# Kernel tuning notes

Measured on AMD Instinct MI355X. Metric: run time of the kernel, lower is better.

Reference implementation:

```python
import jax, jax.numpy as jnp
import numpy as np

B, N, C, H = 2, 2048, 1024, 16
D = C // H
SCALE = D ** -0.5


def setup_inputs() -> dict:
    key = jax.random.key(0)
    ks = jax.random.split(key, 5)
    x = jax.random.normal(ks[0], (B, N, C), dtype=jnp.float32)
    # causal mask, broadcast over batch: True = attend
    attention_mask = jnp.broadcast_to(jnp.tril(jnp.ones((N, N), dtype=bool)), (B, N, N))
    w_qkv = jax.random.normal(ks[1], (3 * C, C), dtype=jnp.float32) * (C ** -0.5)
    b_qkv = jax.random.normal(ks[2], (3 * C,), dtype=jnp.float32) * 0.02
    w_proj = jax.random.normal(ks[3], (C, C), dtype=jnp.float32) * (C ** -0.5)
    b_proj = jax.random.normal(ks[4], (C,), dtype=jnp.float32) * 0.02
    return {"x": x, "attention_mask": attention_mask, "w_qkv": w_qkv,
            "b_qkv": b_qkv, "w_proj": w_proj, "b_proj": b_proj}


def reference(x, attention_mask, w_qkv, b_qkv, w_proj, b_proj):
    b, n, c = x.shape
    qkv = x @ w_qkv.T + b_qkv                      # [B,N,3C]
    qkv = qkv.reshape(b, n, 3, H, D).transpose(2, 0, 3, 1, 4)  # [3,B,H,N,D]
    q, k, v = qkv[0], qkv[1], qkv[2]
    dots = jnp.einsum('bhid,bhjd->bhij', q, k) * SCALE
    mask_value = -jnp.finfo(dots.dtype).max
    dots = jnp.where(attention_mask[:, None, :, :], dots, mask_value)
    attn = jax.nn.softmax(dots.astype(jnp.float32), axis=-1).astype(dots.dtype)
    out = jnp.einsum('bhij,bhjd->bhid', attn, v)   # [B,H,N,D]
    # NOTE: original code reshapes WITHOUT transposing heads back - faithful.
    out = out.reshape(b, n, c)
    return out @ w_proj.T + b_proj
```

## Files before the change

kernel.cpp:

```cpp
#include <hip/hip_runtime.h>
#include <hip/hip_bf16.h>
#include <stdint.h>

#define SL_F 0.18033688011112043f

typedef unsigned short u16;
typedef unsigned int u32;
typedef __attribute__((ext_vector_type(8))) short bf16x8;
typedef __attribute__((ext_vector_type(4))) float f32x4;

__device__ __forceinline__ u16 f2bf(float f) {
    union { float f; u32 u; } v; v.f = f;
    return (u16)((v.u + 0x7fffu + ((v.u >> 16) & 1u)) >> 16);
}
__device__ __forceinline__ u32 pack2bf(float a, float b) {
    union { __hip_bfloat162 h; u32 u; } p;
    p.h = __float22bfloat162_rn(make_float2(a, b));
    return p.u;
}

__device__ __forceinline__ void gl_lds16(const u16* g, u16* l) {
    __builtin_amdgcn_global_load_lds(
        (const __attribute__((address_space(1))) u32*)g,
        (__attribute__((address_space(3))) u32*)l, 16, 0, 0);
}

__global__ __launch_bounds__(256) void convert_k(
    const float4* __restrict__ x, const float4* __restrict__ w1,
    const float4* __restrict__ w2,
    ushort4* __restrict__ xb, ushort4* __restrict__ w1b, ushort4* __restrict__ w2b)
{
    const int i = blockIdx.x * 256 + threadIdx.x;
    const int XN = 4096 * 1024 / 4, W1 = 3072 * 1024 / 4;
    float4 v; ushort4* dst;
    if (i < XN)            { v = x[i];            dst = &xb[i]; }
    else if (i < XN + W1)  { v = w1[i - XN];      dst = &w1b[i - XN]; }
    else                   { v = w2[i - XN - W1]; dst = &w2b[i - XN - W1]; }
    ushort4 o;
    o.x = f2bf(v.x); o.y = f2bf(v.y); o.z = f2bf(v.z); o.w = f2bf(v.w);
    *dst = o;
}

template<int NT, int EPI>
__global__ __launch_bounds__(256) void gemm_nt(
    const u16* __restrict__ A, const u16* __restrict__ Bw,
    const float* __restrict__ bias,
    u16* __restrict__ Qb, u16* __restrict__ Kb, u16* __restrict__ VTb,
    float* __restrict__ Out)
{
    constexpr int NBF = NT / 32;
    constexpr int BGRP = NT / 16;
    __shared__ __align__(16) u16 Al[2][8 * 512];
    __shared__ __align__(16) u16 Bl[2][BGRP * 512];
    const int tid = threadIdx.x;
    const int lane = tid & 63;
    const int w = tid >> 6;
    const int la = lane & 15, qd = lane >> 4;
    const int K = 1024;
    const int m0 = blockIdx.y * 128;
    const int n0 = blockIdx.x * NT;
    const int wm = (w >> 1) * 64, wn = (w & 1) * (NT / 2);

    const u16* Ag0 = A + (size_t)(m0 + (2 * w) * 16 + la) * K + qd * 8;
    const u16* Ag1 = A + (size_t)(m0 + (2 * w + 1) * 16 + la) * K + qd * 8;
    const int bg0 = (BGRP == 8) ? 2 * w : w;
    const u16* Bg0 = Bw + (size_t)(n0 + bg0 * 16 + la) * K + qd * 8;
    const u16* Bg1 = Bw + (size_t)(n0 + (2 * w + 1) * 16 + la) * K + qd * 8;

    auto stage = [&](int k0, int b) {
        gl_lds16(Ag0 + k0, &Al[b][(2 * w) * 512]);
        gl_lds16(Ag1 + k0, &Al[b][(2 * w + 1) * 512]);
        gl_lds16(Bg0 + k0, &Bl[b][bg0 * 512]);
        if (BGRP == 8)
            gl_lds16(Bg1 + k0, &Bl[b][(2 * w + 1) * 512]);
    };

    f32x4 acc[4][NBF] = {};
    int buf = 0;
    stage(0, 0);

    for (int k0 = 0; k0 < K; k0 += 32) {
        __syncthreads();
        if (k0 + 32 < K) stage(k0 + 32, buf ^ 1);

        bf16x8 af[4], bfr[NBF];
#pragma unroll
        for (int i = 0; i < 4; i++)
            af[i] = *(const bf16x8*)&Al[buf][(((unsigned)wm >> 4) + i) * 512 + lane * 8];
#pragma unroll
        for (int j = 0; j < NBF; j++)
            bfr[j] = *(const bf16x8*)&Bl[buf][(((unsigned)wn >> 4) + j) * 512 + lane * 8];
#pragma unroll
        for (int i = 0; i < 4; i++)
#pragma unroll
            for (int j = 0; j < NBF; j++)
                acc[i][j] = __builtin_amdgcn_mfma_f32_16x16x32_bf16(
                    af[i], bfr[j], acc[i][j], 0, 0, 0);
        buf ^= 1;
    }

#pragma unroll
    for (int j = 0; j < NBF; j++) {
        const int col = n0 + wn + j * 16 + la;
        const float bv = bias[col];
        if (EPI == 0) {
            const int t = col >> 10, hd = col & 1023, h = hd >> 6, d = hd & 63;
#pragma unroll
            for (int i = 0; i < 4; i++)
#pragma unroll
                for (int r = 0; r < 4; r++) {
                    const int row = m0 + wm + i * 16 + qd * 4 + r;
                    const int b = row >> 11, n = row & 2047;
                    const int bh = b * 16 + h;
                    const u16 val = f2bf(acc[i][j][r] + bv);
                    if (t == 0)      Qb[((size_t)bh * 2048 + n) * 64 + d] = val;
                    else if (t == 1) Kb[((size_t)bh * 2048 + n) * 64 + d] = val;
                    else             VTb[((size_t)bh * 64 + d) * 2048 + n] = val;
                }
        } else {
#pragma unroll
            for (int i = 0; i < 4; i++)
#pragma unroll
                for (int r = 0; r < 4; r++) {
                    const int row = m0 + wm + i * 16 + qd * 4 + r;
                    Out[(size_t)row * 1024 + col] = acc[i][j][r] + bv;
                }
        }
    }
}

__global__ __launch_bounds__(256) void attn_k(
    const u16* __restrict__ Qb, const u16* __restrict__ Kb,
    const u16* __restrict__ VTb, u16* __restrict__ Ob)
{
    __shared__ __align__(16) u16 Kl[2][16 * 512];
    __shared__ __align__(16) u16 Vl[2][16 * 512];
    __shared__ __align__(16) u16 Pl[4][16 * 72];
    const int bh = blockIdx.x & 31;
    const int pair = blockIdx.x >> 5;
    const int tid = threadIdx.x;
    const int lane = tid & 63;
    const int w = tid >> 6;
    const int la = lane & 15, qd = lane >> 4;

    const u16* Kbase = Kb + (size_t)bh * 2048 * 64;
    const u16* Vbase = VTb + (size_t)bh * 64 * 2048;
    u16* Pw = &Pl[w][0];

    u32 ksrc[4], vsrc[4];
#pragma unroll
    for (int t = 0; t < 4; t++) {
        const int ck = 4 * w + t;
        ksrc[t] = (u32)((ck >> 1) * 16 + la) * 64 + (ck & 1) * 32 + qd * 8;
        vsrc[t] = (u32)((ck >> 2) * 16 + la) * 2048 + (ck & 3) * 32 + qd * 8;
    }
    auto stage = [&](int j0, int b) {
#pragma unroll
        for (int t = 0; t < 4; t++) {
            gl_lds16(Kbase + (u32)j0 * 64 + ksrc[t], &Kl[b][(4 * w + t) * 512]);
            gl_lds16(Vbase + (u32)j0 + vsrc[t], &Vl[b][(4 * w + t) * 512]);
        }
    };

    int buf = 0;
    stage(0, 0);

    for (int half = 0; half < 2; half++) {
        const int tile = (half == 0) ? pair : 31 - pair;
        const int q0 = tile * 64 + w * 16;
        const int jmax = (tile >> 1) * 128;
        const int qrow = q0 + la;

        const u16* Qp = Qb + ((size_t)bh * 2048 + q0 + la) * 64 + qd * 8;
        const bf16x8 qf0 = *(const bf16x8*)Qp;
        const bf16x8 qf1 = *(const bf16x8*)(Qp + 32);

        f32x4 o[4] = {};
        float lsum = 0.f;

        for (int j0 = 0; j0 <= jmax; j0 += 128) {
            __syncthreads();

            const int nj = (j0 + 128 <= jmax) ? (j0 + 128) : ((half == 0) ? 0 : -1);
            if (nj >= 0) stage(nj, buf ^ 1);

            f32x4 s[8];
#pragma unroll
            for (int c = 0; c < 8; c++) {
                f32x4 z = {};
                const bf16x8 kf0 = *(const bf16x8*)&Kl[buf][(c * 2 + 0) * 512 + lane * 8];
                const bf16x8 kf1 = *(const bf16x8*)&Kl[buf][(c * 2 + 1) * 512 + lane * 8];
                z = __builtin_amdgcn_mfma_f32_16x16x32_bf16(kf0, qf0, z, 0, 0, 0);
                z = __builtin_amdgcn_mfma_f32_16x16x32_bf16(kf1, qf1, z, 0, 0, 0);
                s[c] = z;
            }

            if (j0 == jmax) {
#pragma unroll
                for (int c = 0; c < 8; c++)
#pragma unroll
                    for (int r = 0; r < 4; r++) {
                        const int j = j0 + c * 16 + qd * 4 + r;
                        float v = s[c][r] * SL_F;
                        v = (j > qrow) ? -1e30f : v;
                        s[c][r] = __builtin_amdgcn_exp2f(v);
                    }
            } else {
#pragma unroll
                for (int c = 0; c < 8; c++)
#pragma unroll
                    for (int r = 0; r < 4; r++)
                        s[c][r] = __builtin_amdgcn_exp2f(s[c][r] * SL_F);
            }
#pragma unroll
            for (int c = 0; c < 8; c++)
#pragma unroll
                for (int r = 0; r < 4; r++)
                    lsum += s[c][r];

#pragma unroll
            for (int hh = 0; hh < 2; hh++) {
#pragma unroll
                for (int c = 0; c < 4; c++) {
                    uint2 pw;
                    pw.x = pack2bf(s[hh * 4 + c][0], s[hh * 4 + c][1]);
                    pw.y = pack2bf(s[hh * 4 + c][2], s[hh * 4 + c][3]);
                    *(uint2*)&Pw[la * 72 + c * 16 + qd * 4] = pw;
                }
                const bf16x8 pf0 = *(const bf16x8*)&Pw[la * 72 + qd * 8];
                const bf16x8 pf1 = *(const bf16x8*)&Pw[la * 72 + 32 + qd * 8];
#pragma unroll
                for (int c2 = 0; c2 < 4; c2++) {
                    const bf16x8 vf0 = *(const bf16x8*)&Vl[buf][(c2 * 4 + hh * 2 + 0) * 512 + lane * 8];
                    const bf16x8 vf1 = *(const bf16x8*)&Vl[buf][(c2 * 4 + hh * 2 + 1) * 512 + lane * 8];
                    o[c2] = __builtin_amdgcn_mfma_f32_16x16x32_bf16(pf0, vf0, o[c2], 0, 0, 0);
                    o[c2] = __builtin_amdgcn_mfma_f32_16x16x32_bf16(pf1, vf1, o[c2], 0, 0, 0);
                }
            }
            buf ^= 1;
        }

        lsum += __shfl_xor(lsum, 16, 64);
        lsum += __shfl_xor(lsum, 32, 64);
        float rinv[4];
#pragma unroll
        for (int r = 0; r < 4; r++)
            rinv[r] = 1.0f / __shfl(lsum, qd * 4 + r, 64);

        u16* Op = Ob + (size_t)bh * 2048 * 64;
#pragma unroll
        for (int c2 = 0; c2 < 4; c2++)
#pragma unroll
            for (int r = 0; r < 4; r++) {
                const int row = q0 + qd * 4 + r;
                Op[(size_t)row * 64 + c2 * 16 + la] = f2bf(o[c2][r] * rinv[r]);
            }
    }
}

extern "C" void kernel_launch(void* const* d_in, const int* in_sizes, int n_in,
                              void* d_out, int out_size, void* d_ws, size_t ws_size,
                              hipStream_t stream)
{
    const float* x     = (const float*)d_in[0];
    const float* wqkv  = (const float*)d_in[2];
    const float* bqkv  = (const float*)d_in[3];
    const float* wproj = (const float*)d_in[4];
    const float* bproj = (const float*)d_in[5];
    float* out = (float*)d_out;

    u16* ws     = (u16*)d_ws;
    u16* xb     = ws;
    u16* wqkvb  = xb + 4096 * 1024;
    u16* wprojb = wqkvb + 3072 * 1024;
    u16* Qb     = wprojb + 1024 * 1024;
    u16* Kb     = Qb + 32 * 2048 * 64;
    u16* VTb    = Kb + 32 * 2048 * 64;
    u16* Ob     = VTb + 32 * 2048 * 64;

    convert_k<<<dim3(8192), dim3(256), 0, stream>>>(
        (const float4*)x, (const float4*)wqkv, (const float4*)wproj,
        (ushort4*)xb, (ushort4*)wqkvb, (ushort4*)wprojb);

    gemm_nt<128, 0><<<dim3(24, 32), dim3(256), 0, stream>>>(
        xb, wqkvb, bqkv, Qb, Kb, VTb, (float*)nullptr);

    attn_k<<<dim3(512), dim3(256), 0, stream>>>(Qb, Kb, VTb, Ob);

    gemm_nt<64, 1><<<dim3(16, 32), dim3(256), 0, stream>>>(
        Ob, wprojb, bproj, (u16*)nullptr, (u16*)nullptr, (u16*)nullptr, out);
}
```

Baseline: 229.4 us.

## Replace QKV GEMM with 256x256-tile, 512-thread, 4-stage pipelined kernel

```diff
diff --git a/kernel.cpp b/kernel.cpp
--- a/kernel.cpp
+++ b/kernel.cpp
@@ -39,6 +39,97 @@
     ushort4 o;
     o.x = f2bf(v.x); o.y = f2bf(v.y); o.z = f2bf(v.z); o.w = f2bf(v.w);
     *dst = o;
+}
+
+__global__ __launch_bounds__(512) void gemm256_qkv(
+    const u16* __restrict__ A, const u16* __restrict__ Bw,
+    const float* __restrict__ bias,
+    u16* __restrict__ Qb, u16* __restrict__ Kb, u16* __restrict__ VTb)
+{
+    __shared__ __align__(16) u16 Al[4][16 * 512];
+    __shared__ __align__(16) u16 Bl[4][16 * 512];
+    const int tid = threadIdx.x;
+    const int lane = tid & 63;
+    const int w = tid >> 6;
+    const int la = lane & 15, qd = lane >> 4;
+
+    const int bid = blockIdx.x;
+    const int xcd = bid & 7, ci = bid >> 3;
+    const int m0 = ((xcd >> 1) * 4 + ci / 6) * 256;
+    const int n0 = ((xcd & 1) * 6 + ci % 6) * 256;
+
+    const int wrow = (w >> 2) * 8;
+    const int wcol = (w & 3) * 4;
+
+    const u16* Ag0 = A + (size_t)(m0 + w * 16 + la) * 1024 + qd * 8;
+    const u16* Ag1 = Ag0 + (size_t)128 * 1024;
+    const u16* Bg0 = Bw + (size_t)(n0 + w * 16 + la) * 1024 + qd * 8;
+    const u16* Bg1 = Bg0 + (size_t)128 * 1024;
+
+    auto stage = [&](int kt, int b) {
+        const int k0 = kt * 32;
+        gl_lds16(Ag0 + k0, &Al[b][w * 512]);
+        gl_lds16(Ag1 + k0, &Al[b][(8 + w) * 512]);
+        gl_lds16(Bg0 + k0, &Bl[b][w * 512]);
+        gl_lds16(Bg1 + k0, &Bl[b][(8 + w) * 512]);
+    };
+
+    f32x4 acc[8][4] = {};
+
+    auto comp = [&](int b) {
+        bf16x8 af[8], bfr[4];
+#pragma unroll
+        for (int i = 0; i < 8; i++)
+            af[i] = *(const bf16x8*)&Al[b][(wrow + i) * 512 + lane * 8];
+#pragma unroll
+        for (int j = 0; j < 4; j++)
+            bfr[j] = *(const bf16x8*)&Bl[b][(wcol + j) * 512 + lane * 8];
+        __builtin_amdgcn_s_setprio(1);
+#pragma unroll
+        for (int i = 0; i < 8; i++)
+#pragma unroll
+            for (int j = 0; j < 4; j++)
+                acc[i][j] = __builtin_amdgcn_mfma_f32_16x16x32_bf16(
+                    af[i], bfr[j], acc[i][j], 0, 0, 0);
+        __builtin_amdgcn_s_setprio(0);
+    };
+
+    stage(0, 0); stage(1, 1); stage(2, 2);
+
+    for (int kt = 0; kt < 30; ++kt) {
+        asm volatile("s_waitcnt vmcnt(8)" ::: "memory");
+        __builtin_amdgcn_s_barrier();
+        asm volatile("" ::: "memory");
+        if (kt < 29) stage(kt + 3, (kt + 3) & 3);
+        comp(kt & 3);
+    }
+    asm volatile("s_waitcnt vmcnt(4)" ::: "memory");
+    __builtin_amdgcn_s_barrier();
+    asm volatile("" ::: "memory");
+    comp(30 & 3);
+    asm volatile("s_waitcnt vmcnt(0)" ::: "memory");
+    __builtin_amdgcn_s_barrier();
+    asm volatile("" ::: "memory");
+    comp(31 & 3);
+
+#pragma unroll
+    for (int jn = 0; jn < 4; jn++) {
+        const int col = n0 + (w & 3) * 64 + jn * 16 + la;
+        const float bv = bias[col];
+        const int t = col >> 10, hd = col & 1023, h = hd >> 6, d = hd & 63;
+#pragma unroll
+        for (int i = 0; i < 8; i++)
+#pragma unroll
+            for (int r = 0; r < 4; r++) {
+                const int row = m0 + (w >> 2) * 128 + i * 16 + qd * 4 + r;
+                const int bb = row >> 11, n = row & 2047;
+                const int bh = bb * 16 + h;
+                const u16 val = f2bf(acc[i][jn][r] + bv);
+                if (t == 0)      Qb[((size_t)bh * 2048 + n) * 64 + d] = val;
+                else if (t == 1) Kb[((size_t)bh * 2048 + n) * 64 + d] = val;
+                else             VTb[((size_t)bh * 64 + d) * 2048 + n] = val;
+            }
+    }
 }
 
 template<int NT, int EPI>
@@ -282,8 +373,8 @@
         (const float4*)x, (const float4*)wqkv, (const float4*)wproj,
         (ushort4*)xb, (ushort4*)wqkvb, (ushort4*)wprojb);
 
-    gemm_nt<128, 0><<<dim3(24, 32), dim3(256), 0, stream>>>(
-        xb, wqkvb, bqkv, Qb, Kb, VTb, (float*)nullptr);
+    gemm256_qkv<<<dim3(192), dim3(512), 0, stream>>>(
+        xb, wqkvb, bqkv, Qb, Kb, VTb);
 
     attn_k<<<dim3(512), dim3(256), 0, stream>>>(Qb, Kb, VTb, Ob);
 
```

Result: slower. 251.1 us (+9.5%).
